# Performance work log

Measured on AMD Instinct MI355X. Metric: run time of the kernel, lower is better.

The kernel has to match this reference:

```python
import jax, jax.numpy as jnp
import numpy as np

D_MODEL = 384
KSIZE = 3
B, L = 32, 512
LN_EPS = 1e-5


def _conv1d_same(x, w, b):
    # x: [B, C_in, L], w: [C_out, C_in, K] -> [B, C_out, L]
    y = jax.lax.conv_general_dilated(
        x, w, window_strides=(1,), padding='SAME',
        dimension_numbers=('NCH', 'OIH', 'NCH'))
    return y + b[None, :, None]


def _conv_fft_block(x, wa, ba, wb, bb):
    # Conv1D_FFT: transpose -> conv/relu -> conv/relu -> transpose back
    h = jnp.transpose(x, (0, 2, 1))            # [B, D, L]
    h = jax.nn.relu(_conv1d_same(h, wa, ba))
    h = jax.nn.relu(_conv1d_same(h, wb, bb))
    return jnp.transpose(h, (0, 2, 1))         # [B, L, D]


def _layernorm(x, g, b):
    mu = jnp.mean(x, axis=-1, keepdims=True)
    var = jnp.var(x, axis=-1, keepdims=True)
    return (x - mu) * jax.lax.rsqrt(var + LN_EPS) * g + b


def setup_inputs() -> dict:
    key = jax.random.key(0)
    ks = jax.random.split(key, 8)
    x = jax.random.normal(ks[0], (B, L, D_MODEL), dtype=jnp.float32)
    durations = jax.random.randint(ks[1], (B, L), 0, 8, dtype=jnp.int32)
    s = 0.02
    params = {
        'c1a_w': jax.random.normal(ks[2], (D_MODEL, D_MODEL, KSIZE), jnp.float32) * s,
        'c1a_b': jnp.zeros((D_MODEL,), jnp.float32),
        'c1b_w': jax.random.normal(ks[3], (D_MODEL, D_MODEL, KSIZE), jnp.float32) * s,
        'c1b_b': jnp.zeros((D_MODEL,), jnp.float32),
        'ln1_g': jnp.ones((D_MODEL,), jnp.float32),
        'ln1_b': jnp.zeros((D_MODEL,), jnp.float32),
        'c2a_w': jax.random.normal(ks[4], (D_MODEL, D_MODEL, KSIZE), jnp.float32) * s,
        'c2a_b': jnp.zeros((D_MODEL,), jnp.float32),
        'c2b_w': jax.random.normal(ks[5], (D_MODEL, D_MODEL, KSIZE), jnp.float32) * s,
        'c2b_b': jnp.zeros((D_MODEL,), jnp.float32),
        'ln2_g': jnp.ones((D_MODEL,), jnp.float32),
        'ln2_b': jnp.zeros((D_MODEL,), jnp.float32),
        'lin_w': jax.random.normal(ks[6], (D_MODEL, 1), jnp.float32) * s,
        'lin_b': jnp.zeros((1,), jnp.float32),
    }
    return {'x': x, 'durations': durations, **params}


def reference(x, durations, c1a_w, c1a_b, c1b_w, c1b_b, ln1_g, ln1_b,
              c2a_w, c2a_b, c2b_w, c2b_b, ln2_g, ln2_b, lin_w, lin_b):
    # --- DurationPredictor (dropout = identity, eval mode) ---
    h = _conv_fft_block(x, c1a_w, c1a_b, c1b_w, c1b_b)
    h = _layernorm(h, ln1_g, ln1_b)
    h = _conv_fft_block(h, c2a_w, c2a_b, c2b_w, c2b_b)
    h = _layernorm(h, ln2_g, ln2_b)
    dur_preds = (h @ lin_w + lin_b)[..., 0]      # [B, L]

    # --- LR: duration-based expansion via one-hot alignment matmul ---
    total = jnp.sum(durations, axis=-1)          # [B]
    T = int(jnp.max(total))                      # concrete (durations are input data)
    cum = jnp.cumsum(durations, axis=-1)         # [B, L]
    t = jnp.arange(T, dtype=cum.dtype)           # [T]
    # frame t belongs to phoneme j s.t. cum[j-1] <= t < cum[j]
    idx = jax.vmap(lambda c: jnp.searchsorted(c, t, side='right'))(cum)  # [B, T]
    mask = (t[None, :] < total[:, None]).astype(x.dtype)                 # [B, T]
    align = jax.nn.one_hot(idx, x.shape[1], dtype=x.dtype) * mask[:, :, None]  # [B, T, L]
    out = jnp.einsum('btl,bld->btd', align, x)   # [B, T, D]
    return (out, dur_preds)
```

## Files before the change

### kernel.cpp

```cpp
#include <hip/hip_runtime.h>

#define B_   32
#define L_   512
#define D_   384
#define M_   (B_*L_)
#define KTOT (D_*3)
#define LDW  392
#define BROWS 82
#define BUFE (BROWS*LDW)

typedef __bf16 bf16x8 __attribute__((ext_vector_type(8)));
typedef float  floatx4 __attribute__((ext_vector_type(4)));

__global__ __launch_bounds__(256) void repack4_kernel(const float* __restrict__ wa,
                                                      const float* __restrict__ wb,
                                                      const float* __restrict__ wc,
                                                      const float* __restrict__ wd,
                                                      __bf16* __restrict__ oa,
                                                      __bf16* __restrict__ ob,
                                                      __bf16* __restrict__ oc,
                                                      __bf16* __restrict__ od)
{
    int idx = blockIdx.x * 256 + threadIdx.x;
    if (idx >= D_ * KTOT) return;
    const float* w; __bf16* o_;
    switch (blockIdx.y) {
        case 0:  w = wa; o_ = oa; break;
        case 1:  w = wb; o_ = ob; break;
        case 2:  w = wc; o_ = oc; break;
        default: w = wd; o_ = od; break;
    }
    int j  = idx & 7;
    int l  = (idx >> 3) & 63;
    int ct = idx >> 9;
    int c  = ct / 24;
    int t  = ct - c * 24;
    int o  = t * 16 + (l & 15);
    int kflat = c * 32 + (l >> 4) * 8 + j;
    int s  = kflat / D_;
    int i  = kflat - s * D_;
    o_[idx] = (__bf16)w[(o * D_ + i) * 3 + s];
}

__global__ __launch_bounds__(512, 1) void fused_predictor(
    const float* __restrict__ x,
    const __bf16* __restrict__ w1a, const float* __restrict__ b1a,
    const __bf16* __restrict__ w1b, const float* __restrict__ b1b,
    const float* __restrict__ g1,  const float* __restrict__ e1,
    const __bf16* __restrict__ w2a, const float* __restrict__ b2a,
    const __bf16* __restrict__ w2b, const float* __restrict__ b2b,
    const float* __restrict__ g2,  const float* __restrict__ e2,
    const float* __restrict__ lw,  const float* __restrict__ lb,
    float* __restrict__ out_dur)
{
    extern __shared__ char smem_raw[];
    __bf16* bufA = (__bf16*)smem_raw;
    __bf16* bufB = bufA + BUFE;
    float*  red1 = (float*)(bufB + BUFE);
    float*  red2 = red1 + BROWS * 8;
    float*  minv = red2 + BROWS * 8;

    const int m0 = blockIdx.x * 64;
    const int l0 = m0 & 511;
    const int b0 = m0 - l0;

    const int tid  = threadIdx.x;
    const int wave = tid >> 6;
    const int lane = tid & 63;
    const int quad = lane >> 4;
    const int lx   = lane & 15;
    const int ng   = wave & 3;
    const int mg   = wave >> 2;
    const int mtc  = mg ? 2 : 3;
    const int mtb  = mg ? 3 : 0;

    bf16x8 kz;
#pragma unroll
    for (int z = 0; z < 8; z++) kz[z] = (__bf16)0.f;

    for (int c = tid; c < BROWS * 48; c += 512) {
        int beta = c / 48, q = c - beta * 48;
        int l = l0 + beta - 9;
        bf16x8 v = kz;
        if ((unsigned)l < (unsigned)L_) {
            const float* xr = x + (size_t)(b0 + l) * D_ + q * 8;
            const float4 f0 = *(const float4*)xr;
            const float4 f1 = *(const float4*)(xr + 4);
            v[0] = (__bf16)f0.x; v[1] = (__bf16)f0.y; v[2] = (__bf16)f0.z; v[3] = (__bf16)f0.w;
            v[4] = (__bf16)f1.x; v[5] = (__bf16)f1.y; v[6] = (__bf16)f1.z; v[7] = (__bf16)f1.w;
        }
        *(bf16x8*)(&bufA[beta * LDW + q * 8]) = v;
    }
    for (int c = tid; c < 2 * 48; c += 512) {
        int beta = (c < 48) ? 0 : 81, q = c % 48;
        *(bf16x8*)(&bufB[beta * LDW + q * 8]) = kz;
    }
    __syncthreads();

    const int t0   = ng * 6;
    const int col0 = ng * 96 + lx;

    floatx4 acc[3][6];
    bf16x8  bg[3][6];

    for (int st = 0; st < 4; st++) {
        const __bf16* bin  = (st & 1) ? bufB : bufA;
        __bf16*       bout = (st & 1) ? bufA : bufB;
        const __bf16* Wp = (st == 0) ? w1a : (st == 1) ? w1b : (st == 2) ? w2a : w2b;
        const float*  bp = (st == 0) ? b1a : (st == 1) ? b1b : (st == 2) ? b2a : b2b;

#pragma unroll
        for (int mt = 0; mt < 3; mt++)
            if (mt < mtc)
#pragma unroll
                for (int ni = 0; ni < 6; ni++)
#pragma unroll
                    for (int r = 0; r < 4; r++) acc[mt][ni][r] = 0.f;

        const char* pb0 = (const char*)Wp + ((size_t)t0 * 64 + lane) * 16;
        auto loadB = [&](int buf, int n) {
            int it = n / 3, s = n - it * 3;
            const char* p = pb0 + (size_t)(s * 12 + it) * 24576;
#pragma unroll
            for (int ni = 0; ni < 6; ni++)
                bg[buf][ni] = *(const bf16x8*)(p + ni * 1024);
        };
        loadB(0, 0); loadB(1, 1);

        const __bf16* ab = bin + (mtb * 16 + lx) * LDW + quad * 8;
#pragma unroll
        for (int n = 0; n < 36; n++) {
            const int it = n / 3, s = n - it * 3;
            if (n + 2 < 36) loadB((n + 2) % 3, n + 2);
            bf16x8 af[3];
            af[0] = *(const bf16x8*)(ab + (s) * LDW + it * 32);
            af[1] = *(const bf16x8*)(ab + (16 + s) * LDW + it * 32);
            if (mtc == 3)
                af[2] = *(const bf16x8*)(ab + (32 + s) * LDW + it * 32);
            __builtin_amdgcn_s_setprio(1);
#pragma unroll
            for (int ni = 0; ni < 6; ni++) {
                acc[0][ni] = __builtin_amdgcn_mfma_f32_16x16x32_bf16(af[0], bg[n % 3][ni], acc[0][ni], 0, 0, 0);
                acc[1][ni] = __builtin_amdgcn_mfma_f32_16x16x32_bf16(af[1], bg[n % 3][ni], acc[1][ni], 0, 0, 0);
            }
            if (mtc == 3) {
#pragma unroll
                for (int ni = 0; ni < 6; ni++)
                    acc[2][ni] = __builtin_amdgcn_mfma_f32_16x16x32_bf16(af[2], bg[n % 3][ni], acc[2][ni], 0, 0, 0);
            }
            __builtin_amdgcn_s_setprio(0);
        }

        float bv[6];
#pragma unroll
        for (int ni = 0; ni < 6; ni++) bv[ni] = bp[col0 + ni * 16];
#pragma unroll
        for (int mt = 0; mt < 3; mt++)
            if (mt < mtc)
#pragma unroll
                for (int ni = 0; ni < 6; ni++)
#pragma unroll
                    for (int r = 0; r < 4; r++) {
                        float vv = acc[mt][ni][r] + bv[ni];
                        acc[mt][ni][r] = vv > 0.f ? vv : 0.f;
                    }

        if (st == 1 || st == 3) {
#pragma unroll
            for (int mt = 0; mt < 3; mt++)
                if (mt < mtc)
#pragma unroll
                    for (int r = 0; r < 4; r++) {
                        float s1 = 0.f, s2 = 0.f;
#pragma unroll
                        for (int ni = 0; ni < 6; ni++) {
                            s1 += acc[mt][ni][r];
                            s2 += acc[mt][ni][r] * acc[mt][ni][r];
                        }
#pragma unroll
                        for (int d = 1; d < 16; d <<= 1) {
                            s1 += __shfl_xor(s1, d);
                            s2 += __shfl_xor(s2, d);
                        }
                        if (lx == 0) {
                            int beta = (mtb + mt) * 16 + quad * 4 + r + 1;
                            red1[beta * 8 + wave] = s1;
                            red2[beta * 8 + wave] = s2;
                        }
                    }
            __syncthreads();
            if (tid < BROWS) {
                int tile = (tid - 1) >> 4;
                int base = (tile >= 3) ? 4 : 0;
                float s1 = 0.f, s2 = 0.f;
#pragma unroll
                for (int k = 0; k < 4; k++) { s1 += red1[tid * 8 + base + k]; s2 += red2[tid * 8 + base + k]; }
                float mean = s1 * (1.f / D_);
                float var  = s2 * (1.f / D_) - mean * mean;
                minv[tid * 2]     = mean;
                minv[tid * 2 + 1] = rsqrtf(var + 1e-5f);
            }
            __syncthreads();
            const float* gp = (st == 1) ? g1 : g2;
            const float* ep = (st == 1) ? e1 : e2;
            float gv[6], ev[6];
#pragma unroll
            for (int ni = 0; ni < 6; ni++) { gv[ni] = gp[col0 + ni * 16]; ev[ni] = ep[col0 + ni * 16]; }
#pragma unroll
            for (int mt = 0; mt < 3; mt++)
                if (mt < mtc)
#pragma unroll
                    for (int r = 0; r < 4; r++) {
                        int beta = (mtb + mt) * 16 + quad * 4 + r + 1;
                        float mean = minv[beta * 2], inv = minv[beta * 2 + 1];
#pragma unroll
                        for (int ni = 0; ni < 6; ni++)
                            acc[mt][ni][r] = (acc[mt][ni][r] - mean) * inv * gv[ni] + ev[ni];
                    }
            if (st == 1) {
#pragma unroll
                for (int mt = 0; mt < 3; mt++)
                    if (mt < mtc)
#pragma unroll
                        for (int r = 0; r < 4; r++) {
                            int beta = (mtb + mt) * 16 + quad * 4 + r + 1;
                            bool ok = (unsigned)(l0 + beta - 9) < (unsigned)L_;
#pragma unroll
                            for (int ni = 0; ni < 6; ni++)
                                bout[beta * LDW + col0 + ni * 16] = (__bf16)(ok ? acc[mt][ni][r] : 0.f);
                        }
            } else {
                float lwv[6];
#pragma unroll
                for (int ni = 0; ni < 6; ni++) lwv[ni] = lw[col0 + ni * 16];
#pragma unroll
                for (int mt = 0; mt < 3; mt++)
                    if (mt < mtc)
#pragma unroll
                        for (int r = 0; r < 4; r++) {
                            float p = 0.f;
#pragma unroll
                            for (int ni = 0; ni < 6; ni++) p += acc[mt][ni][r] * lwv[ni];
#pragma unroll
                            for (int d = 1; d < 16; d <<= 1) p += __shfl_xor(p, d);
                            if (lx == 0) {
                                int beta = (mtb + mt) * 16 + quad * 4 + r + 1;
                                red1[beta * 8 + wave] = p;
                            }
                        }
                __syncthreads();
                if (tid < 64) {
                    int beta = tid + 9;
                    int tile = (beta - 1) >> 4;
                    int base = (tile >= 3) ? 4 : 0;
                    float sacc = lb[0];
#pragma unroll
                    for (int k = 0; k < 4; k++) sacc += red1[beta * 8 + base + k];
                    out_dur[m0 + tid] = sacc;
                }
            }
        } else {
#pragma unroll
            for (int mt = 0; mt < 3; mt++)
                if (mt < mtc)
#pragma unroll
                    for (int r = 0; r < 4; r++) {
                        int beta = (mtb + mt) * 16 + quad * 4 + r + 1;
                        bool ok = (unsigned)(l0 + beta - 9) < (unsigned)L_;
#pragma unroll
                        for (int ni = 0; ni < 6; ni++)
                            bout[beta * LDW + col0 + ni * 16] = (__bf16)(ok ? acc[mt][ni][r] : 0.f);
                    }
        }
        __syncthreads();
    }
}

__global__ __launch_bounds__(64) void cum_kernel(const int* __restrict__ dur,
                                                 int* __restrict__ cum)
{
    int b = blockIdx.x, lane = threadIdx.x;
    const int* db = dur + b * L_;
    int v[8], s = 0;
#pragma unroll
    for (int i = 0; i < 8; i++) { v[i] = db[lane * 8 + i]; s += v[i]; }
    int ex = s;
#pragma unroll
    for (int off = 1; off < 64; off <<= 1) {
        int n = __shfl_up(ex, off);
        if (lane >= off) ex += n;
    }
    ex -= s;
    int c = ex;
    int* cb = cum + b * L_;
#pragma unroll
    for (int i = 0; i < 8; i++) { c += v[i]; cb[lane * 8 + i] = c; }
}

__global__ __launch_bounds__(128) void scatter_kernel(const float* __restrict__ x,
                                                      const int* __restrict__ cum,
                                                      float* __restrict__ out, int T)
{
    int pl = blockIdx.x;
    int b  = pl >> 9;
    int l  = pl & (L_ - 1);
    const int* cb = cum + b * L_;
    int e = cb[l];
    int s = l ? cb[l - 1] : 0;
    if (e == s) return;
    int tid = threadIdx.x;
    float4 v = make_float4(0.f, 0.f, 0.f, 0.f);
    if (tid < 96) v = *(const float4*)(x + (size_t)pl * D_ + tid * 4);
    float* ob = out + ((size_t)b * T) * D_ + tid * 4;
    if (tid < 96)
        for (int t = s; t < e; ++t)
            *(float4*)(ob + (size_t)t * D_) = v;
}

__global__ __launch_bounds__(256) void ztail_kernel(const int* __restrict__ cum,
                                                    float* __restrict__ out, int T)
{
    int b = blockIdx.y;
    int total = cum[b * L_ + L_ - 1];
    int nfr = T - total;
    if (nfr <= 0) return;
    float* base = out + ((size_t)b * T + total) * D_;
    int n4 = nfr * 96;
    for (int i = blockIdx.x * 256 + threadIdx.x; i < n4; i += gridDim.x * 256) {
        int fr = i / 96, q = i - fr * 96;
        *(float4*)(base + (size_t)fr * D_ + q * 4) = make_float4(0.f, 0.f, 0.f, 0.f);
    }
}

extern "C" void kernel_launch(void* const* d_in, const int* in_sizes, int n_in,
                              void* d_out, int out_size, void* d_ws, size_t ws_size,
                              hipStream_t stream) {
    const float* x       = (const float*)d_in[0];
    const int*   dur     = (const int*)d_in[1];
    const float* c1a_w   = (const float*)d_in[2];
    const float* c1a_b   = (const float*)d_in[3];
    const float* c1b_w   = (const float*)d_in[4];
    const float* c1b_b   = (const float*)d_in[5];
    const float* ln1_g   = (const float*)d_in[6];
    const float* ln1_b   = (const float*)d_in[7];
    const float* c2a_w   = (const float*)d_in[8];
    const float* c2a_b   = (const float*)d_in[9];
    const float* c2b_w   = (const float*)d_in[10];
    const float* c2b_b   = (const float*)d_in[11];
    const float* ln2_g   = (const float*)d_in[12];
    const float* ln2_b   = (const float*)d_in[13];
    const float* lin_w   = (const float*)d_in[14];
    const float* lin_b   = (const float*)d_in[15];

    const int T = (out_size - B_ * L_) / (B_ * D_);
    float* out_gather = (float*)d_out;
    float* out_dur    = (float*)d_out + (size_t)B_ * T * D_;

    char* p = (char*)d_ws;
    __bf16* w1a = (__bf16*)p; p += (size_t)D_ * KTOT * 2;
    __bf16* w1b = (__bf16*)p; p += (size_t)D_ * KTOT * 2;
    __bf16* w2a = (__bf16*)p; p += (size_t)D_ * KTOT * 2;
    __bf16* w2b = (__bf16*)p; p += (size_t)D_ * KTOT * 2;
    int* cum = (int*)p; p += (size_t)B_ * L_ * 4;

    cum_kernel<<<B_, 64, 0, stream>>>(dur, cum);
    scatter_kernel<<<B_ * L_, 128, 0, stream>>>(x, cum, out_gather, T);
    ztail_kernel<<<dim3(16, B_), 256, 0, stream>>>(cum, out_gather, T);

    dim3 rpgrid((D_ * KTOT + 255) / 256, 4);
    repack4_kernel<<<rpgrid, 256, 0, stream>>>(c1a_w, c1b_w, c2a_w, c2b_w, w1a, w1b, w2a, w2b);

    const size_t smem = (size_t)2 * BUFE * 2 + (BROWS * 8 * 2 + BROWS * 2) * 4;
    static bool attr_set = false;
    if (!attr_set) {
        hipFuncSetAttribute((const void*)fused_predictor,
                            hipFuncAttributeMaxDynamicSharedMemorySize, (int)smem);
        attr_set = true;
    }
    fused_predictor<<<256, 512, smem, stream>>>(
        x, w1a, c1a_b, w1b, c1b_b, ln1_g, ln1_b,
        w2a, c2a_b, w2b, c2b_b, ln2_g, ln2_b,
        lin_w, lin_b, out_dur);
}
```

Before: 249.7 us.

## Add 16-wave fused predictor variant splitting M tiles across two wave groups

Adds a 1024-thread version of the fused conv/layernorm predictor kernel. Waves are split into two M-groups, handling 3 and 2 row tiles, times 8 N-groups, which raises the wave count per CU and cuts per-wave MFMA work and register pressure. The reduction buffers grow to 16 slots per row. At runtime the kernel checks the compiled register count and falls back to the 8-wave kernel if it exceeds 128. Risks include spills, more LDS traffic from redundant B-fragment loads, and load imbalance between the two M-groups.

```diff
diff --git a/kernel.cpp b/kernel.cpp
--- a/kernel.cpp
+++ b/kernel.cpp
@@ -42,7 +42,241 @@
     o_[idx] = (__bf16)w[(o * D_ + i) * 3 + s];
 }
 
-__global__ __launch_bounds__(512, 1) void fused_predictor(
+__global__ __launch_bounds__(1024, 2) void fused_predictor16(
+    const float* __restrict__ x,
+    const __bf16* __restrict__ w1a, const float* __restrict__ b1a,
+    const __bf16* __restrict__ w1b, const float* __restrict__ b1b,
+    const float* __restrict__ g1,  const float* __restrict__ e1,
+    const __bf16* __restrict__ w2a, const float* __restrict__ b2a,
+    const __bf16* __restrict__ w2b, const float* __restrict__ b2b,
+    const float* __restrict__ g2,  const float* __restrict__ e2,
+    const float* __restrict__ lw,  const float* __restrict__ lb,
+    float* __restrict__ out_dur)
+{
+    extern __shared__ char smem_raw[];
+    __bf16* bufA = (__bf16*)smem_raw;
+    __bf16* bufB = bufA + BUFE;
+    float*  red1 = (float*)(bufB + BUFE);
+    float*  red2 = red1 + BROWS * 16;
+    float*  minv = red2 + BROWS * 16;
+
+    const int m0 = blockIdx.x * 64;
+    const int l0 = m0 & 511;
+    const int b0 = m0 - l0;
+
+    const int tid  = threadIdx.x;
+    const int wave = tid >> 6;
+    const int lane = tid & 63;
+    const int quad = lane >> 4;
+    const int lx   = lane & 15;
+    const int ng   = wave & 7;
+    const int mg   = wave >> 3;
+    const int mtc  = mg ? 2 : 3;
+    const int mtb  = mg ? 3 : 0;
+
+    bf16x8 kz;
+#pragma unroll
+    for (int z = 0; z < 8; z++) kz[z] = (__bf16)0.f;
+
+    for (int c = tid; c < BROWS * 48; c += 1024) {
+        int beta = c / 48, q = c - beta * 48;
+        int l = l0 + beta - 9;
+        bf16x8 v = kz;
+        if ((unsigned)l < (unsigned)L_) {
+            const float* xr = x + (size_t)(b0 + l) * D_ + q * 8;
+            const float4 f0 = *(const float4*)xr;
+            const float4 f1 = *(const float4*)(xr + 4);
+            v[0] = (__bf16)f0.x; v[1] = (__bf16)f0.y; v[2] = (__bf16)f0.z; v[3] = (__bf16)f0.w;
+            v[4] = (__bf16)f1.x; v[5] = (__bf16)f1.y; v[6] = (__bf16)f1.z; v[7] = (__bf16)f1.w;
+        }
+        *(bf16x8*)(&bufA[beta * LDW + q * 8]) = v;
+    }
+    for (int c = tid; c < 2 * 48; c += 1024) {
+        int beta = (c < 48) ? 0 : 81, q = c % 48;
+        *(bf16x8*)(&bufB[beta * LDW + q * 8]) = kz;
+    }
+    __syncthreads();
+
+    const int t0   = ng * 3;
+    const int col0 = ng * 48 + lx;
+
+    floatx4 acc[3][3];
+    bf16x8  bg[3][3];
+
+    for (int st = 0; st < 4; st++) {
+        const __bf16* bin  = (st & 1) ? bufB : bufA;
+        __bf16*       bout = (st & 1) ? bufA : bufB;
+        const __bf16* Wp = (st == 0) ? w1a : (st == 1) ? w1b : (st == 2) ? w2a : w2b;
+        const float*  bp = (st == 0) ? b1a : (st == 1) ? b1b : (st == 2) ? b2a : b2b;
+
+#pragma unroll
+        for (int mt = 0; mt < 3; mt++)
+            if (mt < mtc)
+#pragma unroll
+                for (int ni = 0; ni < 3; ni++)
+#pragma unroll
+                    for (int r = 0; r < 4; r++) acc[mt][ni][r] = 0.f;
+
+        const char* pb0 = (const char*)Wp + ((size_t)t0 * 64 + lane) * 16;
+        auto loadB = [&](int buf, int n) {
+            int it = n / 3, s = n - it * 3;
+            const char* p = pb0 + (size_t)(s * 12 + it) * 24576;
+#pragma unroll
+            for (int ni = 0; ni < 3; ni++)
+                bg[buf][ni] = *(const bf16x8*)(p + ni * 1024);
+        };
+        loadB(0, 0); loadB(1, 1);
+
+        const __bf16* ab = bin + (mtb * 16 + lx) * LDW + quad * 8;
+#pragma unroll
+        for (int n = 0; n < 36; n++) {
+            const int it = n / 3, s = n - it * 3;
+            if (n + 2 < 36) loadB((n + 2) % 3, n + 2);
+            bf16x8 af[3];
+            af[0] = *(const bf16x8*)(ab + (s) * LDW + it * 32);
+            af[1] = *(const bf16x8*)(ab + (16 + s) * LDW + it * 32);
+            if (mtc == 3)
+                af[2] = *(const bf16x8*)(ab + (32 + s) * LDW + it * 32);
+            __builtin_amdgcn_s_setprio(1);
+#pragma unroll
+            for (int ni = 0; ni < 3; ni++) {
+                acc[0][ni] = __builtin_amdgcn_mfma_f32_16x16x32_bf16(af[0], bg[n % 3][ni], acc[0][ni], 0, 0, 0);
+                acc[1][ni] = __builtin_amdgcn_mfma_f32_16x16x32_bf16(af[1], bg[n % 3][ni], acc[1][ni], 0, 0, 0);
+            }
+            if (mtc == 3) {
+#pragma unroll
+                for (int ni = 0; ni < 3; ni++)
+                    acc[2][ni] = __builtin_amdgcn_mfma_f32_16x16x32_bf16(af[2], bg[n % 3][ni], acc[2][ni], 0, 0, 0);
+            }
+            __builtin_amdgcn_s_setprio(0);
+        }
+
+        float bv[3];
+#pragma unroll
+        for (int ni = 0; ni < 3; ni++) bv[ni] = bp[col0 + ni * 16];
+#pragma unroll
+        for (int mt = 0; mt < 3; mt++)
+            if (mt < mtc)
+#pragma unroll
+                for (int ni = 0; ni < 3; ni++)
+#pragma unroll
+                    for (int r = 0; r < 4; r++) {
+                        float vv = acc[mt][ni][r] + bv[ni];
+                        acc[mt][ni][r] = vv > 0.f ? vv : 0.f;
+                    }
+
+        if (st == 1 || st == 3) {
+#pragma unroll
+            for (int mt = 0; mt < 3; mt++)
+                if (mt < mtc)
+#pragma unroll
+                    for (int r = 0; r < 4; r++) {
+                        float s1 = 0.f, s2 = 0.f;
+#pragma unroll
+                        for (int ni = 0; ni < 3; ni++) {
+                            s1 += acc[mt][ni][r];
+                            s2 += acc[mt][ni][r] * acc[mt][ni][r];
+                        }
+#pragma unroll
+                        for (int d = 1; d < 16; d <<= 1) {
+                            s1 += __shfl_xor(s1, d);
+                            s2 += __shfl_xor(s2, d);
+                        }
+                        if (lx == 0) {
+                            int beta = (mtb + mt) * 16 + quad * 4 + r + 1;
+                            red1[beta * 16 + wave] = s1;
+                            red2[beta * 16 + wave] = s2;
+                        }
+                    }
+            __syncthreads();
+            if (tid < BROWS) {
+                int tile = (tid - 1) >> 4;
+                int base = (tile >= 3) ? 8 : 0;
+                float s1 = 0.f, s2 = 0.f;
+#pragma unroll
+                for (int k = 0; k < 8; k++) { s1 += red1[tid * 16 + base + k]; s2 += red2[tid * 16 + base + k]; }
+                float mean = s1 * (1.f / D_);
+                float var  = s2 * (1.f / D_) - mean * mean;
+                minv[tid * 2]     = mean;
+                minv[tid * 2 + 1] = rsqrtf(var + 1e-5f);
+            }
+            __syncthreads();
+            const float* gp = (st == 1) ? g1 : g2;
+            const float* ep = (st == 1) ? e1 : e2;
+            float gv[3], ev[3];
+#pragma unroll
+            for (int ni = 0; ni < 3; ni++) { gv[ni] = gp[col0 + ni * 16]; ev[ni] = ep[col0 + ni * 16]; }
+#pragma unroll
+            for (int mt = 0; mt < 3; mt++)
+                if (mt < mtc)
+#pragma unroll
+                    for (int r = 0; r < 4; r++) {
+                        int beta = (mtb + mt) * 16 + quad * 4 + r + 1;
+                        float mean = minv[beta * 2], inv = minv[beta * 2 + 1];
+#pragma unroll
+                        for (int ni = 0; ni < 3; ni++)
+                            acc[mt][ni][r] = (acc[mt][ni][r] - mean) * inv * gv[ni] + ev[ni];
+                    }
+            if (st == 1) {
+#pragma unroll
+                for (int mt = 0; mt < 3; mt++)
+                    if (mt < mtc)
+#pragma unroll
+                        for (int r = 0; r < 4; r++) {
+                            int beta = (mtb + mt) * 16 + quad * 4 + r + 1;
+                            bool ok = (unsigned)(l0 + beta - 9) < (unsigned)L_;
+#pragma unroll
+                            for (int ni = 0; ni < 3; ni++)
+                                bout[beta * LDW + col0 + ni * 16] = (__bf16)(ok ? acc[mt][ni][r] : 0.f);
+                        }
+            } else {
+                float lwv[3];
+#pragma unroll
+                for (int ni = 0; ni < 3; ni++) lwv[ni] = lw[col0 + ni * 16];
+#pragma unroll
+                for (int mt = 0; mt < 3; mt++)
+                    if (mt < mtc)
+#pragma unroll
+                        for (int r = 0; r < 4; r++) {
+                            float p = 0.f;
+#pragma unroll
+                            for (int ni = 0; ni < 3; ni++) p += acc[mt][ni][r] * lwv[ni];
+#pragma unroll
+                            for (int d = 1; d < 16; d <<= 1) p += __shfl_xor(p, d);
+                            if (lx == 0) {
+                                int beta = (mtb + mt) * 16 + quad * 4 + r + 1;
+                                red1[beta * 16 + wave] = p;
+                            }
+                        }
+                __syncthreads();
+                if (tid < 64) {
+                    int beta = tid + 9;
+                    int tile = (beta - 1) >> 4;
+                    int base = (tile >= 3) ? 8 : 0;
+                    float sacc = lb[0];
+#pragma unroll
+                    for (int k = 0; k < 8; k++) sacc += red1[beta * 16 + base + k];
+                    out_dur[m0 + tid] = sacc;
+                }
+            }
+        } else {
+#pragma unroll
+            for (int mt = 0; mt < 3; mt++)
+                if (mt < mtc)
+#pragma unroll
+                    for (int r = 0; r < 4; r++) {
+                        int beta = (mtb + mt) * 16 + quad * 4 + r + 1;
+                        bool ok = (unsigned)(l0 + beta - 9) < (unsigned)L_;
+#pragma unroll
+                        for (int ni = 0; ni < 3; ni++)
+                            bout[beta * LDW + col0 + ni * 16] = (__bf16)(ok ? acc[mt][ni][r] : 0.f);
+                    }
+        }
+        __syncthreads();
+    }
+}
+
+__global__ __launch_bounds__(512, 1) void fused_predictor8(
     const float* __restrict__ x,
     const __bf16* __restrict__ w1a, const float* __restrict__ b1a,
     const __bf16* __restrict__ w1b, const float* __restrict__ b1b,
@@ -370,15 +604,30 @@
     dim3 rpgrid((D_ * KTOT + 255) / 256, 4);
     repack4_kernel<<<rpgrid, 256, 0, stream>>>(c1a_w, c1b_w, c2a_w, c2b_w, w1a, w1b, w2a, w2b);
 
-    const size_t smem = (size_t)2 * BUFE * 2 + (BROWS * 8 * 2 + BROWS * 2) * 4;
-    static bool attr_set = false;
-    if (!attr_set) {
-        hipFuncSetAttribute((const void*)fused_predictor,
-                            hipFuncAttributeMaxDynamicSharedMemorySize, (int)smem);
-        attr_set = true;
-    }
-    fused_predictor<<<256, 512, smem, stream>>>(
-        x, w1a, c1a_b, w1b, c1b_b, ln1_g, ln1_b,
-        w2a, c2a_b, w2b, c2b_b, ln2_g, ln2_b,
-        lin_w, lin_b, out_dur);
+    const size_t smem8  = (size_t)2 * BUFE * 2 + (BROWS * 8  * 2 + BROWS * 2) * 4;
+    const size_t smem16 = (size_t)2 * BUFE * 2 + (BROWS * 16 * 2 + BROWS * 2) * 4;
+
+    static int use16 = -1;
+    if (use16 < 0) {
+        hipFuncSetAttribute((const void*)fused_predictor8,
+                            hipFuncAttributeMaxDynamicSharedMemorySize, (int)smem8);
+        hipFuncSetAttribute((const void*)fused_predictor16,
+                            hipFuncAttributeMaxDynamicSharedMemorySize, (int)smem16);
+        hipFuncAttributes fa{};
+        use16 = 0;
+        if (hipFuncGetAttributes(&fa, (const void*)fused_predictor16) == hipSuccess &&
+            fa.numRegs > 0 && fa.numRegs <= 128)
+            use16 = 1;
+    }
+
+    if (use16)
+        fused_predictor16<<<256, 1024, smem16, stream>>>(
+            x, w1a, c1a_b, w1b, c1b_b, ln1_g, ln1_b,
+            w2a, c2a_b, w2b, c2b_b, ln2_g, ln2_b,
+            lin_w, lin_b, out_dur);
+    else
+        fused_predictor8<<<256, 512, smem8, stream>>>(
+            x, w1a, c1a_b, w1b, c1b_b, ln1_g, ln1_b,
+            w2a, c2a_b, w2b, c2b_b, ln2_g, ln2_b,
+            lin_w, lin_b, out_dur);
 }
```

New measurement: 263.4 us. +5.5%, slower.
